# Optimization experiments

Hardware: AMD Instinct MI355X
Metric: run time of the kernel (lower is better)

## Reference

```python
import jax, jax.numpy as jnp
import numpy as np

N, E, NG = 20000, 300000, 64
IN_CH, EDGE_DIM = 64, 7
H1, H2, H3 = 128, 64, 32
HEADS = 4
BN_EPS = 1e-5
NEG_SLOPE = 0.2


def _gat_params(key, in_ch, heads, out_ch, concat):
    ks = jax.random.split(key, 6)
    s_in = 1.0 / np.sqrt(in_ch)
    s_e = 1.0 / np.sqrt(EDGE_DIM)
    W = jax.random.uniform(ks[0], (in_ch, heads * out_ch), minval=-s_in, maxval=s_in)
    a_s = jax.random.uniform(ks[1], (heads, out_ch), minval=-s_in, maxval=s_in)
    a_d = jax.random.uniform(ks[2], (heads, out_ch), minval=-s_in, maxval=s_in)
    We = jax.random.uniform(ks[3], (EDGE_DIM, heads * out_ch), minval=-s_e, maxval=s_e)
    a_e = jax.random.uniform(ks[4], (heads, out_ch), minval=-s_e, maxval=s_e)
    b = jnp.zeros((heads * out_ch,) if concat else (out_ch,), jnp.float32)
    return W, a_s, a_d, We, a_e, b


def _bn_params(key, c):
    k1, k2, k3, k4 = jax.random.split(key, 4)
    g = jax.random.uniform(k1, (c,), minval=0.5, maxval=1.5)
    be = jax.random.normal(k2, (c,)) * 0.1
    rm = jax.random.normal(k3, (c,)) * 0.1
    rv = jax.random.uniform(k4, (c,), minval=0.5, maxval=1.5)
    return g, be, rm, rv


def setup_inputs() -> dict:
    key = jax.random.key(0)
    ks = jax.random.split(key, 12)
    inp = {}
    inp["x"] = jax.random.normal(ks[0], (N, IN_CH), dtype=jnp.float32)
    inp["edge_index"] = jax.random.randint(ks[1], (2, E), 0, N)
    inp["edge_attr"] = jax.random.uniform(ks[2], (E, EDGE_DIM), dtype=jnp.float32)
    inp["batch"] = jnp.sort(jax.random.randint(ks[3], (N,), 0, NG))
    inp["w1"], inp["as1"], inp["ad1"], inp["we1"], inp["ae1"], inp["b1"] = _gat_params(ks[4], IN_CH, HEADS, H1, True)
    inp["g1"], inp["bt1"], inp["rm1"], inp["rv1"] = _bn_params(ks[5], H1 * HEADS)
    inp["w2"], inp["as2"], inp["ad2"], inp["we2"], inp["ae2"], inp["b2"] = _gat_params(ks[6], H1 * HEADS, HEADS, H2, True)
    inp["g2"], inp["bt2"], inp["rm2"], inp["rv2"] = _bn_params(ks[7], H2 * HEADS)
    inp["w3"], inp["as3"], inp["ad3"], inp["we3"], inp["ae3"], inp["b3"] = _gat_params(ks[8], H2 * HEADS, 1, H3, False)
    inp["g3"], inp["bt3"], inp["rm3"], inp["rv3"] = _bn_params(ks[9], H3)
    k10a, k10b = jax.random.split(ks[10])
    s = 1.0 / np.sqrt(H3 * 2)
    inp["lw1"] = jax.random.uniform(k10a, (H3 * 2, 32), minval=-s, maxval=s)
    inp["lb1"] = jax.random.uniform(k10b, (32,), minval=-s, maxval=s)
    k11a, k11b = jax.random.split(ks[11])
    s2 = 1.0 / np.sqrt(32)
    inp["lw2"] = jax.random.uniform(k11a, (32, 1), minval=-s2, maxval=s2)
    inp["lb2"] = jax.random.uniform(k11b, (1,), minval=-s2, maxval=s2)
    return inp


def gat_conv(x, src, dst, eattr, W, a_s, a_d, We, a_e, b, heads, out_ch, concat):
    n = x.shape[0]
    # add self loops; edge_attr for loops = per-destination mean of incoming edge_attr (PyG fill_value='mean')
    deg = jax.ops.segment_sum(jnp.ones_like(eattr[:, 0]), dst, num_segments=n)
    loop_attr = jax.ops.segment_sum(eattr, dst, num_segments=n) / jnp.clip(deg, 1.0)[:, None]
    ar = jnp.arange(n)
    s = jnp.concatenate([src, ar])
    d = jnp.concatenate([dst, ar])
    ea = jnp.concatenate([eattr, loop_attr], axis=0)
    h = (x @ W).reshape(n, heads, out_ch)                       # [N,H,C]
    a_src = jnp.sum(h * a_s, axis=-1)                           # [N,H]
    a_dst = jnp.sum(h * a_d, axis=-1)
    ee = (ea @ We).reshape(-1, heads, out_ch)                   # [Etot,H,C]
    a_edge = jnp.sum(ee * a_e, axis=-1)                         # [Etot,H]
    logit = jax.nn.leaky_relu(a_src[s] + a_dst[d] + a_edge, NEG_SLOPE)
    m = jax.ops.segment_max(logit, d, num_segments=n)           # self loops => every node non-empty
    p = jnp.exp(logit - m[d])
    den = jax.ops.segment_sum(p, d, num_segments=n)
    alpha = p / den[d]                                          # [Etot,H]
    msg = (alpha[..., None] * h[s]).reshape(-1, heads * out_ch)
    out = jax.ops.segment_sum(msg, d, num_segments=n)           # [N,H*C]
    if concat:
        return out + b
    return out.reshape(n, heads, out_ch).mean(axis=1) + b


def bn_eval(x, g, be, rm, rv):
    return (x - rm) * (g / jnp.sqrt(rv + BN_EPS)) + be


def reference(x, edge_index, edge_attr, batch,
              w1, as1, ad1, we1, ae1, b1, g1, bt1, rm1, rv1,
              w2, as2, ad2, we2, ae2, b2, g2, bt2, rm2, rv2,
              w3, as3, ad3, we3, ae3, b3, g3, bt3, rm3, rv3,
              lw1, lb1, lw2, lb2):
    src, dst = edge_index[0], edge_index[1]
    h = jax.nn.relu(bn_eval(gat_conv(x, src, dst, edge_attr, w1, as1, ad1, we1, ae1, b1, HEADS, H1, True), g1, bt1, rm1, rv1))
    h = jax.nn.relu(bn_eval(gat_conv(h, src, dst, edge_attr, w2, as2, ad2, we2, ae2, b2, HEADS, H2, True), g2, bt2, rm2, rv2))
    h = jax.nn.relu(bn_eval(gat_conv(h, src, dst, edge_attr, w3, as3, ad3, we3, ae3, b3, 1, H3, False), g3, bt3, rm3, rv3))
    counts = jax.ops.segment_sum(jnp.ones_like(h[:, 0]), batch, num_segments=NG)
    mean_pool = jax.ops.segment_sum(h, batch, num_segments=NG) / jnp.clip(counts, 1.0)[:, None]
    max_pool = jax.ops.segment_max(h, batch, num_segments=NG)
    max_pool = jnp.where(counts[:, None] > 0, max_pool, 0.0)
    z = jnp.concatenate([mean_pool, max_pool], axis=1)          # [NG, 2*H3]
    z = jax.nn.relu(z @ lw1 + lb1)
    return jax.nn.sigmoid(z @ lw2 + lb2).squeeze(-1)            # [NG]
```

## Files before the change

kernel.cpp:

```cpp
#include <hip/hip_runtime.h>
#include <math.h>

#define NEG_SLOPE 0.2f
#define BN_EPS 1e-5f

typedef __attribute__((ext_vector_type(8))) short bf16x8;
typedef __attribute__((ext_vector_type(4))) float f32x4;
typedef unsigned short u16;
typedef __attribute__((ext_vector_type(4))) unsigned short u16x4;

static __device__ __forceinline__ float leaky(float v) { return v > 0.f ? v : NEG_SLOPE * v; }
static __device__ __forceinline__ float b2f(u16 b) { return __uint_as_float(((unsigned)b) << 16); }
static __device__ __forceinline__ u16 f2b(float f) {
  unsigned u = __float_as_uint(f);
  u += 0x7FFF + ((u >> 16) & 1);
  return (u16)(u >> 16);
}
static __device__ __forceinline__ float sel4(f32x4 v, int hs) {
  float a = (hs & 1) ? v[1] : v[0];
  float b = (hs & 1) ? v[3] : v[2];
  return (hs & 2) ? b : a;
}

__global__ void k_prep(const float* __restrict__ W1, const float* __restrict__ W2, const float* __restrict__ W3,
                       const float* __restrict__ AS1, const float* __restrict__ AD1,
                       const float* __restrict__ WE1, const float* __restrict__ AE1,
                       const float* __restrict__ WE2, const float* __restrict__ AE2,
                       const float* __restrict__ WE3, const float* __restrict__ AE3,
                       u16* __restrict__ Wt1, u16* __restrict__ Wt2, u16* __restrict__ Wt3,
                       float* __restrict__ ws1, float* __restrict__ wd1,
                       float* __restrict__ watt1, float* __restrict__ watt2, float* __restrict__ watt3,
                       int* __restrict__ degInt, int* __restrict__ cursor, int Nn) {
  int idx = blockIdx.x * blockDim.x + threadIdx.x;
  if (idx < 32768) {
    int k = idx >> 9, n = idx & 511;
    Wt1[n * 64 + k] = f2b(W1[idx]);
  } else if (idx < 163840) {
    int i = idx - 32768;
    int k = i >> 8, n = i & 255;
    Wt2[n * 512 + k] = f2b(W2[i]);
  } else if (idx < 172032) {
    int i = idx - 163840;
    int k = i >> 5, n = i & 31;
    Wt3[n * 256 + k] = f2b(W3[i]);
  } else if (idx < 172288) {
    int t = idx - 172032;
    int k = t >> 2, h = t & 3;
    float s1 = 0.f, s2 = 0.f;
    for (int c = 0; c < 128; c++) {
      float w = W1[k * 512 + h * 128 + c];
      s1 += w * AS1[h * 128 + c];
      s2 += w * AD1[h * 128 + c];
    }
    ws1[t] = s1; wd1[t] = s2;
  } else if (idx < 172316) {
    int t = idx - 172288;
    int d = t >> 2, h = t & 3;
    float s = 0.f;
    for (int c = 0; c < 128; c++) s += WE1[d * 512 + h * 128 + c] * AE1[h * 128 + c];
    watt1[t] = s;
  } else if (idx < 172344) {
    int t = idx - 172316;
    int d = t >> 2, h = t & 3;
    float s = 0.f;
    for (int c = 0; c < 64; c++) s += WE2[d * 256 + h * 64 + c] * AE2[h * 64 + c];
    watt2[t] = s;
  } else if (idx < 172351) {
    int d = idx - 172344;
    float s = 0.f;
    for (int c = 0; c < 32; c++) s += WE3[d * 32 + c] * AE3[c];
    watt3[d] = s;
  } else if (idx >= 172352 && idx < 172352 + Nn) {
    degInt[idx - 172352] = 0;
  } else if (idx >= 172352 + Nn && idx < 172352 + 2 * Nn) {
    cursor[idx - 172352 - Nn] = 0;
  }
}

__global__ void k_deg(const int* __restrict__ dst, int* __restrict__ degInt, int E) {
  int e = blockIdx.x * blockDim.x + threadIdx.x;
  if (e < E) atomicAdd(&degInt[dst[e]], 1);
}

__global__ void k_scan(const int* __restrict__ degInt, int* __restrict__ rowStart, int n) {
  __shared__ int sums[1024];
  int tid = threadIdx.x;
  int per = (n + 1023) / 1024;
  int start = tid * per;
  int end = start + per; if (end > n) end = n;
  int s = 0;
  for (int i = start; i < end; i++) s += degInt[i];
  sums[tid] = s;
  __syncthreads();
  for (int off = 1; off < 1024; off <<= 1) {
    int v = (tid >= off) ? sums[tid - off] : 0;
    __syncthreads();
    sums[tid] += v;
    __syncthreads();
  }
  int base = (tid > 0) ? sums[tid - 1] : 0;
  for (int i = start; i < end; i++) { rowStart[i] = base; base += degInt[i]; }
  if (tid == 1023) rowStart[n] = sums[1023];
}

__global__ void k_fill_csr(const int* __restrict__ src, const int* __restrict__ dst,
                           const int* __restrict__ rowStart, int* __restrict__ cursor,
                           int* __restrict__ csrSrc, int* __restrict__ csrEid,
                           int* __restrict__ posE, int E) {
  int e = blockIdx.x * blockDim.x + threadIdx.x;
  if (e >= E) return;
  int d = dst[e];
  int pos = rowStart[d] + atomicAdd(&cursor[d], 1);
  csrSrc[pos] = src[e];
  csrEid[pos] = e;
  posE[e] = pos;
}

__global__ void k_loop_gather(const int* __restrict__ rowStart, const int* __restrict__ csrEid,
                              const float* __restrict__ eattr, float* __restrict__ loopAttr, int Nn) {
  int i = blockIdx.x * blockDim.x + threadIdx.x;
  if (i >= Nn * 7) return;
  int n = i / 7, k = i % 7;
  int r0 = rowStart[n], r1 = rowStart[n + 1];
  float s = 0.f;
  for (int j = r0; j < r1; j++) s += eattr[csrEid[j] * 7 + k];
  loopAttr[i] = s / fmaxf((float)(r1 - r0), 1.0f);
}

__global__ __launch_bounds__(256) void k_cast_attn_x(const float* __restrict__ x, u16* __restrict__ xbf,
                                                     const float* __restrict__ ws, const float* __restrict__ wd,
                                                     float* __restrict__ asrc, float* __restrict__ adst, int Nn) {
  int n = blockIdx.x * 4 + (threadIdx.x >> 6);
  if (n >= Nn) return;
  int lane = threadIdx.x & 63;
  float xv = x[(size_t)n * 64 + lane];
  xbf[(size_t)n * 64 + lane] = f2b(xv);
  f32x4 vs = *(const f32x4*)(ws + lane * 4);
  f32x4 vd = *(const f32x4*)(wd + lane * 4);
  f32x4 s1, s2;
#pragma unroll
  for (int h = 0; h < 4; h++) { s1[h] = xv * vs[h]; s2[h] = xv * vd[h]; }
#pragma unroll
  for (int off = 1; off < 64; off <<= 1) {
#pragma unroll
    for (int h = 0; h < 4; h++) { s1[h] += __shfl_xor(s1[h], off); s2[h] += __shfl_xor(s2[h], off); }
  }
  if (lane == 0) {
    *(f32x4*)(asrc + n * 4) = s1;
    *(f32x4*)(adst + n * 4) = s2;
  }
}

template <int BM, int BN, int WM, int WN, bool EPI, int ATTN_H>
__global__ __launch_bounds__(256) void k_gemm_mfma(const u16* __restrict__ A,
                                                   const u16* __restrict__ Bt,
                                                   u16* __restrict__ Cout,
                                                   int M, int K, int Nc, int lda, int ldc,
                                                   int AzOff, int BzOff, int CzOff,
                                                   const float* __restrict__ bias,
                                                   const float* __restrict__ bng,
                                                   const float* __restrict__ bnb,
                                                   const float* __restrict__ bnrm,
                                                   const float* __restrict__ bnrv,
                                                   const float* __restrict__ a_s,
                                                   const float* __restrict__ a_d,
                                                   float* __restrict__ asrc,
                                                   float* __restrict__ adst) {
  constexpr int BK = 64;
  constexpr int LDT = BK + 8;
  __shared__ u16 As[BM][LDT];
  __shared__ u16 Bs[BN][LDT];
  constexpr int NWN = BN / WN;
  constexpr int M_REP = WM / 16;
  constexpr int N_REP = WN / 16;
  int z = blockIdx.z;
  A += (size_t)z * AzOff;
  Bt += (size_t)z * BzOff;
  Cout += (size_t)z * CzOff;
  if (EPI) {
    bias += (size_t)z * CzOff; bng += (size_t)z * CzOff; bnb += (size_t)z * CzOff;
    bnrm += (size_t)z * CzOff; bnrv += (size_t)z * CzOff;
  }
  int tid = threadIdx.x;
  int wid = tid >> 6, lane = tid & 63;
  int wr = wid / NWN, wc = wid % NWN;
  int bm = blockIdx.x * BM, bn = blockIdx.y * BN;
  int l15 = lane & 15, l4 = lane >> 4;

  f32x4 acc[M_REP][N_REP];
#pragma unroll
  for (int m = 0; m < M_REP; m++)
#pragma unroll
    for (int n = 0; n < N_REP; n++) acc[m][n] = (f32x4){0.f, 0.f, 0.f, 0.f};

  for (int k0 = 0; k0 < K; k0 += BK) {
    constexpr int CHA = BM * BK / 8;
#pragma unroll
    for (int ch0 = 0; ch0 < CHA; ch0 += 256) {
      int ch = ch0 + tid;
      int row = ch >> 3, cc = (ch & 7) * 8;
      int gr = bm + row;
      bf16x8 v = {};
      if (gr < M) v = *(const bf16x8*)(A + (size_t)gr * lda + k0 + cc);
      *(bf16x8*)(&As[row][cc]) = v;
    }
    constexpr int CHB = BN * BK / 8;
#pragma unroll
    for (int ch0 = 0; ch0 < CHB; ch0 += 256) {
      int ch = ch0 + tid;
      int row = ch >> 3, cc = (ch & 7) * 8;
      int gr = bn + row;
      bf16x8 v = {};
      if (gr < Nc) v = *(const bf16x8*)(Bt + (size_t)gr * K + k0 + cc);
      *(bf16x8*)(&Bs[row][cc]) = v;
    }
    __syncthreads();
#pragma unroll
    for (int ks = 0; ks < BK; ks += 32) {
      bf16x8 af[M_REP], bfr[N_REP];
#pragma unroll
      for (int m = 0; m < M_REP; m++)
        af[m] = *(const bf16x8*)(&As[wr * WM + m * 16 + l15][ks + l4 * 8]);
#pragma unroll
      for (int n = 0; n < N_REP; n++)
        bfr[n] = *(const bf16x8*)(&Bs[wc * WN + n * 16 + l15][ks + l4 * 8]);
#pragma unroll
      for (int m = 0; m < M_REP; m++)
#pragma unroll
        for (int n = 0; n < N_REP; n++)
          acc[m][n] = __builtin_amdgcn_mfma_f32_16x16x32_bf16(af[m], bfr[n], acc[m][n], 0, 0, 0);
    }
    __syncthreads();
  }
#pragma unroll
  for (int m = 0; m < M_REP; m++) {
#pragma unroll
    for (int r = 0; r < 4; r++) {
      int grow = bm + wr * WM + m * 16 + l4 * 4 + r;
      if (grow >= M) continue;
#pragma unroll
      for (int n = 0; n < N_REP; n++) {
        int gcol = bn + wc * WN + n * 16 + l15;
        if (gcol >= Nc) continue;
        float v = acc[m][n][r];
        if (EPI) {
          v += bias[gcol];
          v = (v - bnrm[gcol]) * (bng[gcol] * rsqrtf(bnrv[gcol] + BN_EPS)) + bnb[gcol];
          v = fmaxf(v, 0.f);
        }
        Cout[(size_t)grow * ldc + gcol] = f2b(v);
      }
    }
  }
  if (ATTN_H > 0) {
    int h = blockIdx.y * NWN + wc;
#pragma unroll
    for (int m = 0; m < M_REP; m++) {
#pragma unroll
      for (int r = 0; r < 4; r++) {
        float s1 = 0.f, s2 = 0.f;
#pragma unroll
        for (int n = 0; n < N_REP; n++) {
          float av = acc[m][n][r];
          int cc = n * 16 + l15;
          s1 += av * a_s[h * WN + cc];
          s2 += av * a_d[h * WN + cc];
        }
#pragma unroll
        for (int off = 1; off < 16; off <<= 1) { s1 += __shfl_xor(s1, off); s2 += __shfl_xor(s2, off); }
        int grow = bm + wr * WM + m * 16 + l4 * 4 + r;
        if (l15 == 0 && grow < M) {
          asrc[grow * ATTN_H + h] = s1;
          adst[grow * ATTN_H + h] = s2;
        }
      }
    }
  }
}

template <int H>
__global__ void k_edge_logit(const int* __restrict__ src, const int* __restrict__ dst,
                             const float* __restrict__ eattr, const int* __restrict__ posE,
                             const float* __restrict__ asrc, const float* __restrict__ adst,
                             const float* __restrict__ w_att, float* __restrict__ logitC, int E) {
  int e = blockIdx.x * blockDim.x + threadIdx.x;
  if (e >= E) return;
  float ea[7];
#pragma unroll
  for (int d = 0; d < 7; d++) ea[d] = eattr[e * 7 + d];
  int s = src[e], dn = dst[e];
  int pos = posE[e];
  if (H == 4) {
    f32x4 va = *(const f32x4*)(asrc + s * 4);
    f32x4 vd = *(const f32x4*)(adst + dn * 4);
    f32x4 o;
#pragma unroll
    for (int h = 0; h < 4; h++) {
      float ae = 0.f;
#pragma unroll
      for (int d = 0; d < 7; d++) ae += ea[d] * w_att[d * 4 + h];
      o[h] = leaky(va[h] + vd[h] + ae);
    }
    *(f32x4*)(logitC + (size_t)pos * 4) = o;
  } else {
    float ae = 0.f;
#pragma unroll
    for (int d = 0; d < 7; d++) ae += ea[d] * w_att[d];
    logitC[pos] = leaky(asrc[s] + adst[dn] + ae);
  }
}

__global__ __launch_bounds__(256) void k_gather_x(
    const int* __restrict__ rowStart, const int* __restrict__ csrSrc,
    const float* __restrict__ logitC, const float* __restrict__ loopAttr,
    const float* __restrict__ w_att, const float* __restrict__ asrc, const float* __restrict__ adst,
    const u16* __restrict__ xbf, u16* __restrict__ aggOut, int Nn) {
  int wid = threadIdx.x >> 6;
  int n = blockIdx.x * 4 + wid;
  if (n >= Nn) return;
  int lane = threadIdx.x & 63;
  __shared__ float pbuf[4][64 * 4];
  int r0 = rowStart[n], r1 = rowStart[n + 1];

  f32x4 va = *(const f32x4*)(asrc + n * 4);
  f32x4 vd = *(const f32x4*)(adst + n * 4);
  float la[7];
#pragma unroll
  for (int d = 0; d < 7; d++) la[d] = loopAttr[n * 7 + d];
  f32x4 ls;
#pragma unroll
  for (int h = 0; h < 4; h++) {
    float ae = 0.f;
#pragma unroll
    for (int d = 0; d < 7; d++) ae += la[d] * w_att[d * 4 + h];
    ls[h] = leaky(va[h] + vd[h] + ae);
  }

  f32x4 m = ls;
  f32x4 denl = {0.f, 0.f, 0.f, 0.f};
  f32x4 acc = {0.f, 0.f, 0.f, 0.f};

  const f32x4* L4 = (const f32x4*)logitC;
  for (int base = r0; base < r1; base += 64) {
    int slot = base + lane;
    bool valid = slot < r1;
    f32x4 lg = valid ? L4[slot] : (f32x4){-1e30f, -1e30f, -1e30f, -1e30f};
    int srcl = valid ? csrSrc[slot] : 0;
    f32x4 mc = lg;
#pragma unroll
    for (int off = 1; off < 64; off <<= 1) {
#pragma unroll
      for (int h = 0; h < 4; h++) mc[h] = fmaxf(mc[h], __shfl_xor(mc[h], off));
    }
    f32x4 rr;
#pragma unroll
    for (int h = 0; h < 4; h++) {
      float mn = fmaxf(m[h], mc[h]);
      rr[h] = __expf(m[h] - mn);
      m[h] = mn;
      denl[h] *= rr[h];
      acc[h] *= rr[h];
    }
    f32x4 ex;
#pragma unroll
    for (int h = 0; h < 4; h++) ex[h] = valid ? __expf(lg[h] - m[h]) : 0.f;
#pragma unroll
    for (int h = 0; h < 4; h++) denl[h] += ex[h];
    *(f32x4*)(&pbuf[wid][lane * 4]) = ex;
    int nv = r1 - base; if (nv > 64) nv = 64;
    int j = 0;
    for (; j + 1 < nv; j += 2) {
      int s0 = __shfl(srcl, j);
      int s1 = __shfl(srcl, j + 1);
      f32x4 p0 = *(const f32x4*)(&pbuf[wid][j * 4]);
      f32x4 p1 = *(const f32x4*)(&pbuf[wid][(j + 1) * 4]);
      float x0 = b2f(xbf[(size_t)s0 * 64 + lane]);
      float x1 = b2f(xbf[(size_t)s1 * 64 + lane]);
#pragma unroll
      for (int h = 0; h < 4; h++) acc[h] += p0[h] * x0 + p1[h] * x1;
    }
    if (j < nv) {
      int s0 = __shfl(srcl, j);
      f32x4 p0 = *(const f32x4*)(&pbuf[wid][j * 4]);
      float x0 = b2f(xbf[(size_t)s0 * 64 + lane]);
#pragma unroll
      for (int h = 0; h < 4; h++) acc[h] += p0[h] * x0;
    }
  }
  f32x4 exs;
#pragma unroll
  for (int h = 0; h < 4; h++) exs[h] = __expf(ls[h] - m[h]);
  f32x4 den;
#pragma unroll
  for (int h = 0; h < 4; h++) {
    float v = denl[h];
#pragma unroll
    for (int off = 1; off < 64; off <<= 1) v += __shfl_xor(v, off);
    den[h] = v + exs[h];
  }
  {
    float xn = b2f(xbf[(size_t)n * 64 + lane]);
#pragma unroll
    for (int h = 0; h < 4; h++) acc[h] += exs[h] * xn;
  }
#pragma unroll
  for (int h = 0; h < 4; h++) pbuf[wid][h * 64 + lane] = acc[h] / den[h];
  u16x4 ov;
#pragma unroll
  for (int jj = 0; jj < 4; jj++) ov[jj] = f2b(pbuf[wid][lane * 4 + jj]);
  *(u16x4*)(aggOut + (size_t)n * 256 + lane * 4) = ov;
}

template <int C, int CPL>
__global__ __launch_bounds__(256) void k_gather4(
    const int* __restrict__ rowStart, const int* __restrict__ csrSrc,
    const float* __restrict__ logitC, const float* __restrict__ loopAttr,
    const float* __restrict__ w_att, const float* __restrict__ asrc, const float* __restrict__ adst,
    const u16* __restrict__ hbuf, const float* __restrict__ bias,
    const float* __restrict__ bng, const float* __restrict__ bnb,
    const float* __restrict__ bnrm, const float* __restrict__ bnrv,
    u16* __restrict__ outbuf, int Nn) {
  constexpr int HC = 4 * C;
  typedef __attribute__((ext_vector_type(CPL))) unsigned short u16v;
  int wid = threadIdx.x >> 6;
  int n = blockIdx.x * 4 + wid;
  if (n >= Nn) return;
  int lane = threadIdx.x & 63;
  int hs = lane >> 4;
  __shared__ float pbuf[4][64 * 4];
  int r0 = rowStart[n], r1 = rowStart[n + 1];

  f32x4 va = *(const f32x4*)(asrc + n * 4);
  f32x4 vd = *(const f32x4*)(adst + n * 4);
  float la[7];
#pragma unroll
  for (int d = 0; d < 7; d++) la[d] = loopAttr[n * 7 + d];
  f32x4 ls;
#pragma unroll
  for (int h = 0; h < 4; h++) {
    float ae = 0.f;
#pragma unroll
    for (int d = 0; d < 7; d++) ae += la[d] * w_att[d * 4 + h];
    ls[h] = leaky(va[h] + vd[h] + ae);
  }

  f32x4 m = ls;
  f32x4 denl = {0.f, 0.f, 0.f, 0.f};
  float acc[CPL];
#pragma unroll
  for (int jj = 0; jj < CPL; jj++) acc[jj] = 0.f;

  const f32x4* L4 = (const f32x4*)logitC;
  for (int base = r0; base < r1; base += 64) {
    int slot = base + lane;
    bool valid = slot < r1;
    f32x4 lg = valid ? L4[slot] : (f32x4){-1e30f, -1e30f, -1e30f, -1e30f};
    int srcl = valid ? csrSrc[slot] : 0;
    f32x4 mc = lg;
#pragma unroll
    for (int off = 1; off < 64; off <<= 1) {
#pragma unroll
      for (int h = 0; h < 4; h++) mc[h] = fmaxf(mc[h], __shfl_xor(mc[h], off));
    }
    f32x4 rr;
#pragma unroll
    for (int h = 0; h < 4; h++) {
      float mn = fmaxf(m[h], mc[h]);
      rr[h] = __expf(m[h] - mn);
      m[h] = mn;
      denl[h] *= rr[h];
    }
    float rrh = sel4(rr, hs);
#pragma unroll
    for (int jj = 0; jj < CPL; jj++) acc[jj] *= rrh;
    f32x4 ex;
#pragma unroll
    for (int h = 0; h < 4; h++) ex[h] = valid ? __expf(lg[h] - m[h]) : 0.f;
#pragma unroll
    for (int h = 0; h < 4; h++) denl[h] += ex[h];
    *(f32x4*)(&pbuf[wid][lane * 4]) = ex;
    int nv = r1 - base; if (nv > 64) nv = 64;
    int j = 0;
    for (; j + 1 < nv; j += 2) {
      int s0 = __shfl(srcl, j);
      int s1 = __shfl(srcl, j + 1);
      float p0 = pbuf[wid][j * 4 + hs];
      float p1 = pbuf[wid][(j + 1) * 4 + hs];
      u16v h0 = *(const u16v*)(hbuf + (size_t)s0 * HC + lane * CPL);
      u16v h1 = *(const u16v*)(hbuf + (size_t)s1 * HC + lane * CPL);
#pragma unroll
      for (int jj = 0; jj < CPL; jj++) acc[jj] += p0 * b2f(h0[jj]) + p1 * b2f(h1[jj]);
    }
    if (j < nv) {
      int s0 = __shfl(srcl, j);
      float p0 = pbuf[wid][j * 4 + hs];
      u16v h0 = *(const u16v*)(hbuf + (size_t)s0 * HC + lane * CPL);
#pragma unroll
      for (int jj = 0; jj < CPL; jj++) acc[jj] += p0 * b2f(h0[jj]);
    }
  }
  f32x4 exs;
#pragma unroll
  for (int h = 0; h < 4; h++) exs[h] = __expf(ls[h] - m[h]);
  f32x4 den;
#pragma unroll
  for (int h = 0; h < 4; h++) {
    float v = denl[h];
#pragma unroll
    for (int off = 1; off < 64; off <<= 1) v += __shfl_xor(v, off);
    den[h] = v + exs[h];
  }
  {
    float ps = sel4(exs, hs);
    u16v hN = *(const u16v*)(hbuf + (size_t)n * HC + lane * CPL);
#pragma unroll
    for (int jj = 0; jj < CPL; jj++) acc[jj] += ps * b2f(hN[jj]);
  }
  float dh = sel4(den, hs);
  u16v ov;
#pragma unroll
  for (int jj = 0; jj < CPL; jj++) {
    int c = lane * CPL + jj;
    float v = acc[jj] / dh + bias[c];
    v = (v - bnrm[c]) * (bng[c] * rsqrtf(bnrv[c] + BN_EPS)) + bnb[c];
    ov[jj] = f2b(fmaxf(v, 0.f));
  }
  *(u16v*)(outbuf + (size_t)n * HC + lane * CPL) = ov;
}

__global__ __launch_bounds__(256) void k_gather_L3(
    const int* __restrict__ rowStart, const int* __restrict__ csrSrc,
    const float* __restrict__ logitC, const float* __restrict__ loopAttr,
    const float* __restrict__ w_att, const float* __restrict__ asrc, const float* __restrict__ adst,
    const u16* __restrict__ hbuf, const float* __restrict__ bias,
    const float* __restrict__ bng, const float* __restrict__ bnb,
    const float* __restrict__ bnrm, const float* __restrict__ bnrv,
    u16* __restrict__ outbuf, int Nn) {
  int n = blockIdx.x * 4 + (threadIdx.x >> 6);
  if (n >= Nn) return;
  int lane = threadIdx.x & 63;
  int cl = lane & 31, half = lane >> 5;
  int r0 = rowStart[n], r1 = rowStart[n + 1];
  float ae = 0.f;
#pragma unroll
  for (int d = 0; d < 7; d++) ae += loopAttr[n * 7 + d] * w_att[d];
  float ls = leaky(asrc[n] + adst[n] + ae);

  float m = ls;
  for (int j = r0 + lane; j < r1; j += 64) m = fmaxf(m, logitC[j]);
  for (int off = 32; off > 0; off >>= 1) m = fmaxf(m, __shfl_xor(m, off));
  float den = 0.f;
  for (int j = r0 + lane; j < r1; j += 64) den += __expf(logitC[j] - m);
  for (int off = 32; off > 0; off >>= 1) den += __shfl_xor(den, off);
  den += __expf(ls - m);

  float acc = 0.f;
  for (int j = r0 + half; j < r1; j += 2) {
    float p = __expf(logitC[j] - m);
    int s = csrSrc[j];
    acc += p * b2f(hbuf[(size_t)s * 32 + cl]);
  }
  if (half == 0) acc += __expf(ls - m) * b2f(hbuf[(size_t)n * 32 + cl]);
  acc += __shfl_xor(acc, 32);
  if (half == 0) {
    float v = acc / den + bias[cl];
    v = (v - bnrm[cl]) * (bng[cl] * rsqrtf(bnrv[cl] + BN_EPS)) + bnb[cl];
    outbuf[(size_t)n * 32 + cl] = f2b(fmaxf(v, 0.f));
  }
}

__global__ __launch_bounds__(256) void k_pool_mlp(
    const u16* __restrict__ h3, const int* __restrict__ batch, int Nn,
    const float* __restrict__ lw1, const float* __restrict__ lb1,
    const float* __restrict__ lw2, const float* __restrict__ lb2,
    float* __restrict__ out) {
  int g = blockIdx.x;
  int tid = threadIdx.x;
  __shared__ int s_lo, s_hi;
  if (tid == 0) {
    int lo = 0, hi = Nn;
    while (lo < hi) { int mid = (lo + hi) >> 1; if (batch[mid] < g) lo = mid + 1; else hi = mid; }
    s_lo = lo;
    int lo2 = lo, hi2 = Nn;
    while (lo2 < hi2) { int mid = (lo2 + hi2) >> 1; if (batch[mid] < g + 1) lo2 = mid + 1; else hi2 = mid; }
    s_hi = lo2;
  }
  __syncthreads();
  int lo = s_lo, hi = s_hi;
  int c = tid & 31, r = tid >> 5;
  float sum = 0.f, mx = -1e30f;
  for (int n = lo + r; n < hi; n += 8) {
    float v = b2f(h3[(size_t)n * 32 + c]);
    sum += v;
    mx = fmaxf(mx, v);
  }
  __shared__ float ssum[8][32];
  __shared__ float smax[8][32];
  ssum[r][c] = sum;
  smax[r][c] = mx;
  __syncthreads();
  __shared__ float z[64];
  __shared__ float zz1[32];
  if (tid < 32) {
    float s = 0.f, m2 = -1e30f;
#pragma unroll
    for (int rr = 0; rr < 8; rr++) { s += ssum[rr][tid]; m2 = fmaxf(m2, smax[rr][tid]); }
    int cnt = hi - lo;
    z[tid] = s / fmaxf((float)cnt, 1.0f);
    z[32 + tid] = (cnt > 0) ? m2 : 0.f;
  }
  __syncthreads();
  if (tid < 32) {
    float s = lb1[tid];
    for (int k = 0; k < 64; k++) s += z[k] * lw1[k * 32 + tid];
    zz1[tid] = fmaxf(s, 0.f);
  }
  __syncthreads();
  if (tid == 0) {
    float s = lb2[0];
    for (int j = 0; j < 32; j++) s += zz1[j] * lw2[j];
    out[g] = 1.f / (1.f + expf(-s));
  }
}

extern "C" void kernel_launch(void* const* d_in, const int* in_sizes, int n_in,
                              void* d_out, int out_size, void* d_ws, size_t ws_size,
                              hipStream_t stream) {
  const float* x     = (const float*)d_in[0];
  const int*   eidx  = (const int*)d_in[1];
  const float* eattr = (const float*)d_in[2];
  const int*   batch = (const int*)d_in[3];
  int N = in_sizes[0] / 64;
  int E = in_sizes[1] / 2;
  int NG = out_size;
  const int* src = eidx;
  const int* dst = eidx + E;

  const float* W[3]  = {(const float*)d_in[4],  (const float*)d_in[14], (const float*)d_in[24]};
  const float* AS[3] = {(const float*)d_in[5],  (const float*)d_in[15], (const float*)d_in[25]};
  const float* AD[3] = {(const float*)d_in[6],  (const float*)d_in[16], (const float*)d_in[26]};
  const float* WE[3] = {(const float*)d_in[7],  (const float*)d_in[17], (const float*)d_in[27]};
  const float* AE[3] = {(const float*)d_in[8],  (const float*)d_in[18], (const float*)d_in[28]};
  const float* B[3]  = {(const float*)d_in[9],  (const float*)d_in[19], (const float*)d_in[29]};
  const float* G[3]  = {(const float*)d_in[10], (const float*)d_in[20], (const float*)d_in[30]};
  const float* BT[3] = {(const float*)d_in[11], (const float*)d_in[21], (const float*)d_in[31]};
  const float* RM[3] = {(const float*)d_in[12], (const float*)d_in[22], (const float*)d_in[32]};
  const float* RV[3] = {(const float*)d_in[13], (const float*)d_in[23], (const float*)d_in[33]};
  const float* lw1 = (const float*)d_in[34];
  const float* lb1 = (const float*)d_in[35];
  const float* lw2 = (const float*)d_in[36];
  const float* lb2 = (const float*)d_in[37];

  char* wp = (char*)d_ws;
  auto alloc = [&](size_t bytes) -> void* {
    void* p = (void*)wp;
    wp += (bytes + 255) & ~(size_t)255;
    return p;
  };
  u16*   xbf      = (u16*)alloc((size_t)N * 64 * 2);
  u16*   aggB     = (u16*)alloc((size_t)N * 256 * 2);
  u16*   bufH     = (u16*)alloc((size_t)N * 512 * 2);
  u16*   bufA     = (u16*)alloc((size_t)N * 512 * 2);
  u16*   Wt1      = (u16*)alloc((size_t)512 * 64 * 2);
  u16*   Wt2      = (u16*)alloc((size_t)256 * 512 * 2);
  u16*   Wt3      = (u16*)alloc((size_t)32 * 256 * 2);
  int*   degInt   = (int*)alloc((size_t)N * 4);
  int*   cursor   = (int*)alloc((size_t)N * 4);
  int*   rowStart = (int*)alloc((size_t)(N + 1) * 4);
  float* loopAttr = (float*)alloc((size_t)N * 7 * 4);
  int*   csrSrc   = (int*)alloc((size_t)E * 4);
  int*   csrEid   = (int*)alloc((size_t)E * 4);
  int*   posE     = (int*)alloc((size_t)E * 4);
  float* logitC   = (float*)alloc((size_t)E * 4 * 4);
  float* asrc     = (float*)alloc((size_t)N * 4 * 4);
  float* adst     = (float*)alloc((size_t)N * 4 * 4);
  float* watt1    = (float*)alloc(28 * 4);
  float* watt2    = (float*)alloc(28 * 4);
  float* watt3    = (float*)alloc(7 * 4);
  float* ws1      = (float*)alloc(64 * 4 * 4);
  float* wd1      = (float*)alloc(64 * 4 * 4);

  int prepTotal = 172352 + 2 * N;
  k_prep<<<(prepTotal + 255) / 256, 256, 0, stream>>>(
      W[0], W[1], W[2], AS[0], AD[0], WE[0], AE[0], WE[1], AE[1], WE[2], AE[2],
      Wt1, Wt2, Wt3, ws1, wd1, watt1, watt2, watt3, degInt, cursor, N);

  k_deg<<<(E + 255) / 256, 256, 0, stream>>>(dst, degInt, E);
  k_scan<<<1, 1024, 0, stream>>>(degInt, rowStart, N);
  k_fill_csr<<<(E + 255) / 256, 256, 0, stream>>>(src, dst, rowStart, cursor, csrSrc, csrEid, posE, E);
  k_loop_gather<<<(N * 7 + 255) / 256, 256, 0, stream>>>(rowStart, csrEid, eattr, loopAttr, N);

  int gmM = (N + 127) / 128;
  int nb4 = (N + 3) / 4;

  k_cast_attn_x<<<nb4, 256, 0, stream>>>(x, xbf, ws1, wd1, asrc, adst, N);
  k_edge_logit<4><<<(E + 255) / 256, 256, 0, stream>>>(src, dst, eattr, posE, asrc, adst, watt1, logitC, E);
  k_gather_x<<<nb4, 256, 0, stream>>>(rowStart, csrSrc, logitC, loopAttr, watt1, asrc, adst, xbf, aggB, N);
  k_gemm_mfma<128, 128, 64, 64, true, 0><<<dim3(gmM, 1, 4), 256, 0, stream>>>(
      aggB, Wt1, bufA, N, 64, 128, 256, 512, 64, 128 * 64, 128,
      B[0], G[0], BT[0], RM[0], RV[0], nullptr, nullptr, nullptr, nullptr);

  k_gemm_mfma<128, 128, 64, 64, false, 4><<<dim3(gmM, 2, 1), 256, 0, stream>>>(
      bufA, Wt2, bufH, N, 512, 256, 512, 256, 0, 0, 0,
      nullptr, nullptr, nullptr, nullptr, nullptr, AS[1], AD[1], asrc, adst);
  k_edge_logit<4><<<(E + 255) / 256, 256, 0, stream>>>(src, dst, eattr, posE, asrc, adst, watt2, logitC, E);
  k_gather4<64, 4><<<nb4, 256, 0, stream>>>(rowStart, csrSrc, logitC, loopAttr, watt2, asrc, adst,
                                            bufH, B[1], G[1], BT[1], RM[1], RV[1], bufA, N);

  k_gemm_mfma<128, 32, 32, 32, false, 1><<<dim3(gmM, 1, 1), 256, 0, stream>>>(
      bufA, Wt3, bufH, N, 256, 32, 256, 32, 0, 0, 0,
      nullptr, nullptr, nullptr, nullptr, nullptr, AS[2], AD[2], asrc, adst);
  k_edge_logit<1><<<(E + 255) / 256, 256, 0, stream>>>(src, dst, eattr, posE, asrc, adst, watt3, logitC, E);
  k_gather_L3<<<nb4, 256, 0, stream>>>(rowStart, csrSrc, logitC, loopAttr, watt3, asrc, adst,
                                       bufH, B[2], G[2], BT[2], RM[2], RV[2], bufA, N);

  k_pool_mlp<<<NG, 256, 0, stream>>>(bufA, batch, N, lw1, lb1, lw2, lb2, (float*)d_out);
}
```

Before: 285.9 us.

## Precompute edge attention terms once and fuse logit computation into gather kernels

Edge-attribute attention projections for all three layers are computed in one pass and stored in CSR order. The three per-layer edge-logit kernels are removed, and each gather kernel now computes logits on the fly from asrc[src], adst[dst] and the precomputed term. The self-loop attribute mean is rebuilt from the per-edge projected terms, which are linear, and folded in at the end with an online-softmax rescale. This drops the loop_gather kernel, the csrEid array and three launches that each wrote and re-read E x 4 logits. In exchange the gathers do an extra dependent load of asrc per edge, and layer 3 is restructured into a single online-softmax pass.

```diff
diff --git a/kernel.cpp b/kernel.cpp
--- a/kernel.cpp
+++ b/kernel.cpp
@@ -105,26 +105,39 @@
 
 __global__ void k_fill_csr(const int* __restrict__ src, const int* __restrict__ dst,
                            const int* __restrict__ rowStart, int* __restrict__ cursor,
-                           int* __restrict__ csrSrc, int* __restrict__ csrEid,
-                           int* __restrict__ posE, int E) {
+                           int* __restrict__ csrSrc, int* __restrict__ posE, int E) {
   int e = blockIdx.x * blockDim.x + threadIdx.x;
   if (e >= E) return;
   int d = dst[e];
   int pos = rowStart[d] + atomicAdd(&cursor[d], 1);
   csrSrc[pos] = src[e];
-  csrEid[pos] = e;
   posE[e] = pos;
 }
 
-__global__ void k_loop_gather(const int* __restrict__ rowStart, const int* __restrict__ csrEid,
-                              const float* __restrict__ eattr, float* __restrict__ loopAttr, int Nn) {
-  int i = blockIdx.x * blockDim.x + threadIdx.x;
-  if (i >= Nn * 7) return;
-  int n = i / 7, k = i % 7;
-  int r0 = rowStart[n], r1 = rowStart[n + 1];
-  float s = 0.f;
-  for (int j = r0; j < r1; j++) s += eattr[csrEid[j] * 7 + k];
-  loopAttr[i] = s / fmaxf((float)(r1 - r0), 1.0f);
+__global__ void k_ae(const float* __restrict__ eattr, const int* __restrict__ posE,
+                     const float* __restrict__ watt1, const float* __restrict__ watt2,
+                     const float* __restrict__ watt3,
+                     float* __restrict__ ae1, float* __restrict__ ae2, float* __restrict__ ae3, int E) {
+  int e = blockIdx.x * blockDim.x + threadIdx.x;
+  if (e >= E) return;
+  float ea[7];
+#pragma unroll
+  for (int d = 0; d < 7; d++) ea[d] = eattr[e * 7 + d];
+  int pos = posE[e];
+  f32x4 o1, o2;
+#pragma unroll
+  for (int h = 0; h < 4; h++) {
+    float a1 = 0.f, a2 = 0.f;
+#pragma unroll
+    for (int d = 0; d < 7; d++) { a1 += ea[d] * watt1[d * 4 + h]; a2 += ea[d] * watt2[d * 4 + h]; }
+    o1[h] = a1; o2[h] = a2;
+  }
+  float a3 = 0.f;
+#pragma unroll
+  for (int d = 0; d < 7; d++) a3 += ea[d] * watt3[d];
+  *(f32x4*)(ae1 + (size_t)pos * 4) = o1;
+  *(f32x4*)(ae2 + (size_t)pos * 4) = o2;
+  ae3[pos] = a3;
 }
 
 __global__ __launch_bounds__(256) void k_cast_attn_x(const float* __restrict__ x, u16* __restrict__ xbf,
@@ -278,42 +291,9 @@
   }
 }
 
-template <int H>
-__global__ void k_edge_logit(const int* __restrict__ src, const int* __restrict__ dst,
-                             const float* __restrict__ eattr, const int* __restrict__ posE,
-                             const float* __restrict__ asrc, const float* __restrict__ adst,
-                             const float* __restrict__ w_att, float* __restrict__ logitC, int E) {
-  int e = blockIdx.x * blockDim.x + threadIdx.x;
-  if (e >= E) return;
-  float ea[7];
-#pragma unroll
-  for (int d = 0; d < 7; d++) ea[d] = eattr[e * 7 + d];
-  int s = src[e], dn = dst[e];
-  int pos = posE[e];
-  if (H == 4) {
-    f32x4 va = *(const f32x4*)(asrc + s * 4);
-    f32x4 vd = *(const f32x4*)(adst + dn * 4);
-    f32x4 o;
-#pragma unroll
-    for (int h = 0; h < 4; h++) {
-      float ae = 0.f;
-#pragma unroll
-      for (int d = 0; d < 7; d++) ae += ea[d] * w_att[d * 4 + h];
-      o[h] = leaky(va[h] + vd[h] + ae);
-    }
-    *(f32x4*)(logitC + (size_t)pos * 4) = o;
-  } else {
-    float ae = 0.f;
-#pragma unroll
-    for (int d = 0; d < 7; d++) ae += ea[d] * w_att[d];
-    logitC[pos] = leaky(asrc[s] + adst[dn] + ae);
-  }
-}
-
 __global__ __launch_bounds__(256) void k_gather_x(
     const int* __restrict__ rowStart, const int* __restrict__ csrSrc,
-    const float* __restrict__ logitC, const float* __restrict__ loopAttr,
-    const float* __restrict__ w_att, const float* __restrict__ asrc, const float* __restrict__ adst,
+    const float* __restrict__ aeC, const float* __restrict__ asrc, const float* __restrict__ adst,
     const u16* __restrict__ xbf, u16* __restrict__ aggOut, int Nn) {
   int wid = threadIdx.x >> 6;
   int n = blockIdx.x * 4 + wid;
@@ -321,31 +301,27 @@
   int lane = threadIdx.x & 63;
   __shared__ float pbuf[4][64 * 4];
   int r0 = rowStart[n], r1 = rowStart[n + 1];
-
-  f32x4 va = *(const f32x4*)(asrc + n * 4);
-  f32x4 vd = *(const f32x4*)(adst + n * 4);
-  float la[7];
-#pragma unroll
-  for (int d = 0; d < 7; d++) la[d] = loopAttr[n * 7 + d];
-  f32x4 ls;
-#pragma unroll
-  for (int h = 0; h < 4; h++) {
-    float ae = 0.f;
-#pragma unroll
-    for (int d = 0; d < 7; d++) ae += la[d] * w_att[d * 4 + h];
-    ls[h] = leaky(va[h] + vd[h] + ae);
-  }
-
-  f32x4 m = ls;
+  f32x4 vaN = *(const f32x4*)(asrc + n * 4);
+  f32x4 vdN = *(const f32x4*)(adst + n * 4);
+
+  f32x4 m = {-1e30f, -1e30f, -1e30f, -1e30f};
   f32x4 denl = {0.f, 0.f, 0.f, 0.f};
+  f32x4 aes = {0.f, 0.f, 0.f, 0.f};
   f32x4 acc = {0.f, 0.f, 0.f, 0.f};
 
-  const f32x4* L4 = (const f32x4*)logitC;
+  const f32x4* AE4 = (const f32x4*)aeC;
   for (int base = r0; base < r1; base += 64) {
     int slot = base + lane;
     bool valid = slot < r1;
-    f32x4 lg = valid ? L4[slot] : (f32x4){-1e30f, -1e30f, -1e30f, -1e30f};
-    int srcl = valid ? csrSrc[slot] : 0;
+    int srcl = 0;
+    f32x4 lg = {-1e30f, -1e30f, -1e30f, -1e30f};
+    if (valid) {
+      srcl = csrSrc[slot];
+      f32x4 vaS = *(const f32x4*)(asrc + srcl * 4);
+      f32x4 ae = AE4[slot];
+#pragma unroll
+      for (int h = 0; h < 4; h++) { aes[h] += ae[h]; lg[h] = leaky(vaS[h] + vdN[h] + ae[h]); }
+    }
     f32x4 mc = lg;
 #pragma unroll
     for (int off = 1; off < 64; off <<= 1) {
@@ -387,9 +363,21 @@
       for (int h = 0; h < 4; h++) acc[h] += p0[h] * x0;
     }
   }
-  f32x4 exs;
-#pragma unroll
-  for (int h = 0; h < 4; h++) exs[h] = __expf(ls[h] - m[h]);
+  float degf = fmaxf((float)(r1 - r0), 1.0f);
+  f32x4 ls, exs;
+#pragma unroll
+  for (int h = 0; h < 4; h++) {
+    float a = aes[h];
+#pragma unroll
+    for (int off = 1; off < 64; off <<= 1) a += __shfl_xor(a, off);
+    ls[h] = leaky(vaN[h] + vdN[h] + a / degf);
+    float mn = fmaxf(m[h], ls[h]);
+    float sc = __expf(m[h] - mn);
+    m[h] = mn;
+    denl[h] *= sc;
+    acc[h] *= sc;
+    exs[h] = __expf(ls[h] - mn);
+  }
   f32x4 den;
 #pragma unroll
   for (int h = 0; h < 4; h++) {
@@ -414,8 +402,7 @@
 template <int C, int CPL>
 __global__ __launch_bounds__(256) void k_gather4(
     const int* __restrict__ rowStart, const int* __restrict__ csrSrc,
-    const float* __restrict__ logitC, const float* __restrict__ loopAttr,
-    const float* __restrict__ w_att, const float* __restrict__ asrc, const float* __restrict__ adst,
+    const float* __restrict__ aeC, const float* __restrict__ asrc, const float* __restrict__ adst,
     const u16* __restrict__ hbuf, const float* __restrict__ bias,
     const float* __restrict__ bng, const float* __restrict__ bnb,
     const float* __restrict__ bnrm, const float* __restrict__ bnrv,
@@ -429,33 +416,29 @@
   int hs = lane >> 4;
   __shared__ float pbuf[4][64 * 4];
   int r0 = rowStart[n], r1 = rowStart[n + 1];
-
-  f32x4 va = *(const f32x4*)(asrc + n * 4);
-  f32x4 vd = *(const f32x4*)(adst + n * 4);
-  float la[7];
-#pragma unroll
-  for (int d = 0; d < 7; d++) la[d] = loopAttr[n * 7 + d];
-  f32x4 ls;
-#pragma unroll
-  for (int h = 0; h < 4; h++) {
-    float ae = 0.f;
-#pragma unroll
-    for (int d = 0; d < 7; d++) ae += la[d] * w_att[d * 4 + h];
-    ls[h] = leaky(va[h] + vd[h] + ae);
-  }
-
-  f32x4 m = ls;
+  f32x4 vaN = *(const f32x4*)(asrc + n * 4);
+  f32x4 vdN = *(const f32x4*)(adst + n * 4);
+
+  f32x4 m = {-1e30f, -1e30f, -1e30f, -1e30f};
   f32x4 denl = {0.f, 0.f, 0.f, 0.f};
+  f32x4 aes = {0.f, 0.f, 0.f, 0.f};
   float acc[CPL];
 #pragma unroll
   for (int jj = 0; jj < CPL; jj++) acc[jj] = 0.f;
 
-  const f32x4* L4 = (const f32x4*)logitC;
+  const f32x4* AE4 = (const f32x4*)aeC;
   for (int base = r0; base < r1; base += 64) {
     int slot = base + lane;
     bool valid = slot < r1;
-    f32x4 lg = valid ? L4[slot] : (f32x4){-1e30f, -1e30f, -1e30f, -1e30f};
-    int srcl = valid ? csrSrc[slot] : 0;
+    int srcl = 0;
+    f32x4 lg = {-1e30f, -1e30f, -1e30f, -1e30f};
+    if (valid) {
+      srcl = csrSrc[slot];
+      f32x4 vaS = *(const f32x4*)(asrc + srcl * 4);
+      f32x4 ae = AE4[slot];
+#pragma unroll
+      for (int h = 0; h < 4; h++) { aes[h] += ae[h]; lg[h] = leaky(vaS[h] + vdN[h] + ae[h]); }
+    }
     f32x4 mc = lg;
 #pragma unroll
     for (int off = 1; off < 64; off <<= 1) {
@@ -499,9 +482,23 @@
       for (int jj = 0; jj < CPL; jj++) acc[jj] += p0 * b2f(h0[jj]);
     }
   }
-  f32x4 exs;
-#pragma unroll
-  for (int h = 0; h < 4; h++) exs[h] = __expf(ls[h] - m[h]);
+  float degf = fmaxf((float)(r1 - r0), 1.0f);
+  f32x4 ls, exs, scv;
+#pragma unroll
+  for (int h = 0; h < 4; h++) {
+    float a = aes[h];
+#pragma unroll
+    for (int off = 1; off < 64; off <<= 1) a += __shfl_xor(a, off);
+    ls[h] = leaky(vaN[h] + vdN[h] + a / degf);
+    float mn = fmaxf(m[h], ls[h]);
+    scv[h] = __expf(m[h] - mn);
+    m[h] = mn;
+    denl[h] *= scv[h];
+    exs[h] = __expf(ls[h] - mn);
+  }
+  float sch = sel4(scv, hs);
+#pragma unroll
+  for (int jj = 0; jj < CPL; jj++) acc[jj] *= sch;
   f32x4 den;
 #pragma unroll
   for (int h = 0; h < 4; h++) {
@@ -530,37 +527,63 @@
 
 __global__ __launch_bounds__(256) void k_gather_L3(
     const int* __restrict__ rowStart, const int* __restrict__ csrSrc,
-    const float* __restrict__ logitC, const float* __restrict__ loopAttr,
-    const float* __restrict__ w_att, const float* __restrict__ asrc, const float* __restrict__ adst,
+    const float* __restrict__ ae3, const float* __restrict__ asrc, const float* __restrict__ adst,
     const u16* __restrict__ hbuf, const float* __restrict__ bias,
     const float* __restrict__ bng, const float* __restrict__ bnb,
     const float* __restrict__ bnrm, const float* __restrict__ bnrv,
     u16* __restrict__ outbuf, int Nn) {
-  int n = blockIdx.x * 4 + (threadIdx.x >> 6);
+  int wid = threadIdx.x >> 6;
+  int n = blockIdx.x * 4 + wid;
   if (n >= Nn) return;
   int lane = threadIdx.x & 63;
   int cl = lane & 31, half = lane >> 5;
+  __shared__ float pbuf[4][64];
   int r0 = rowStart[n], r1 = rowStart[n + 1];
-  float ae = 0.f;
-#pragma unroll
-  for (int d = 0; d < 7; d++) ae += loopAttr[n * 7 + d] * w_att[d];
-  float ls = leaky(asrc[n] + adst[n] + ae);
-
-  float m = ls;
-  for (int j = r0 + lane; j < r1; j += 64) m = fmaxf(m, logitC[j]);
-  for (int off = 32; off > 0; off >>= 1) m = fmaxf(m, __shfl_xor(m, off));
-  float den = 0.f;
-  for (int j = r0 + lane; j < r1; j += 64) den += __expf(logitC[j] - m);
-  for (int off = 32; off > 0; off >>= 1) den += __shfl_xor(den, off);
-  den += __expf(ls - m);
-
-  float acc = 0.f;
-  for (int j = r0 + half; j < r1; j += 2) {
-    float p = __expf(logitC[j] - m);
-    int s = csrSrc[j];
-    acc += p * b2f(hbuf[(size_t)s * 32 + cl]);
-  }
-  if (half == 0) acc += __expf(ls - m) * b2f(hbuf[(size_t)n * 32 + cl]);
+  float vaN = asrc[n], vdN = adst[n];
+
+  float m = -1e30f, denl = 0.f, aes = 0.f, acc = 0.f;
+  for (int base = r0; base < r1; base += 64) {
+    int slot = base + lane;
+    bool valid = slot < r1;
+    int srcl = 0;
+    float lg = -1e30f;
+    if (valid) {
+      srcl = csrSrc[slot];
+      float ae = ae3[slot];
+      aes += ae;
+      lg = leaky(asrc[srcl] + vdN + ae);
+    }
+    float mc = lg;
+#pragma unroll
+    for (int off = 1; off < 64; off <<= 1) mc = fmaxf(mc, __shfl_xor(mc, off));
+    float mn = fmaxf(m, mc);
+    float sc = __expf(m - mn);
+    m = mn;
+    denl *= sc;
+    acc *= sc;
+    float ex = valid ? __expf(lg - m) : 0.f;
+    denl += ex;
+    pbuf[wid][lane] = ex;
+    int nv = r1 - base; if (nv > 64) nv = 64;
+    for (int j = half; j < nv; j += 2) {
+      float p = pbuf[wid][j];
+      int s = __shfl(srcl, j);
+      acc += p * b2f(hbuf[(size_t)s * 32 + cl]);
+    }
+  }
+#pragma unroll
+  for (int off = 1; off < 64; off <<= 1) aes += __shfl_xor(aes, off);
+  float degf = fmaxf((float)(r1 - r0), 1.0f);
+  float ls = leaky(vaN + vdN + aes / degf);
+  float mn = fmaxf(m, ls);
+  float sc = __expf(m - mn);
+  denl *= sc;
+  acc *= sc;
+  float exs = __expf(ls - mn);
+#pragma unroll
+  for (int off = 1; off < 64; off <<= 1) denl += __shfl_xor(denl, off);
+  float den = denl + exs;
+  if (half == 0) acc += exs * b2f(hbuf[(size_t)n * 32 + cl]);
   acc += __shfl_xor(acc, 32);
   if (half == 0) {
     float v = acc / den + bias[cl];
@@ -667,11 +690,11 @@
   int*   degInt   = (int*)alloc((size_t)N * 4);
   int*   cursor   = (int*)alloc((size_t)N * 4);
   int*   rowStart = (int*)alloc((size_t)(N + 1) * 4);
-  float* loopAttr = (float*)alloc((size_t)N * 7 * 4);
   int*   csrSrc   = (int*)alloc((size_t)E * 4);
-  int*   csrEid   = (int*)alloc((size_t)E * 4);
   int*   posE     = (int*)alloc((size_t)E * 4);
-  float* logitC   = (float*)alloc((size_t)E * 4 * 4);
+  float* ae1      = (float*)alloc((size_t)E * 4 * 4);
+  float* ae2      = (float*)alloc((size_t)E * 4 * 4);
+  float* ae3buf   = (float*)alloc((size_t)E * 4);
   float* asrc     = (float*)alloc((size_t)N * 4 * 4);
   float* adst     = (float*)alloc((size_t)N * 4 * 4);
   float* watt1    = (float*)alloc(28 * 4);
@@ -687,15 +710,14 @@
 
   k_deg<<<(E + 255) / 256, 256, 0, stream>>>(dst, degInt, E);
   k_scan<<<1, 1024, 0, stream>>>(degInt, rowStart, N);
-  k_fill_csr<<<(E + 255) / 256, 256, 0, stream>>>(src, dst, rowStart, cursor, csrSrc, csrEid, posE, E);
-  k_loop_gather<<<(N * 7 + 255) / 256, 256, 0, stream>>>(rowStart, csrEid, eattr, loopAttr, N);
+  k_fill_csr<<<(E + 255) / 256, 256, 0, stream>>>(src, dst, rowStart, cursor, csrSrc, posE, E);
+  k_ae<<<(E + 255) / 256, 256, 0, stream>>>(eattr, posE, watt1, watt2, watt3, ae1, ae2, ae3buf, E);
 
   int gmM = (N + 127) / 128;
   int nb4 = (N + 3) / 4;
 
   k_cast_attn_x<<<nb4, 256, 0, stream>>>(x, xbf, ws1, wd1, asrc, adst, N);
-  k_edge_logit<4><<<(E + 255) / 256, 256, 0, stream>>>(src, dst, eattr, posE, asrc, adst, watt1, logitC, E);
-  k_gather_x<<<nb4, 256, 0, stream>>>(rowStart, csrSrc, logitC, loopAttr, watt1, asrc, adst, xbf, aggB, N);
+  k_gather_x<<<nb4, 256, 0, stream>>>(rowStart, csrSrc, ae1, asrc, adst, xbf, aggB, N);
   k_gemm_mfma<128, 128, 64, 64, true, 0><<<dim3(gmM, 1, 4), 256, 0, stream>>>(
       aggB, Wt1, bufA, N, 64, 128, 256, 512, 64, 128 * 64, 128,
       B[0], G[0], BT[0], RM[0], RV[0], nullptr, nullptr, nullptr, nullptr);
@@ -703,15 +725,13 @@
   k_gemm_mfma<128, 128, 64, 64, false, 4><<<dim3(gmM, 2, 1), 256, 0, stream>>>(
       bufA, Wt2, bufH, N, 512, 256, 512, 256, 0, 0, 0,
       nullptr, nullptr, nullptr, nullptr, nullptr, AS[1], AD[1], asrc, adst);
-  k_edge_logit<4><<<(E + 255) / 256, 256, 0, stream>>>(src, dst, eattr, posE, asrc, adst, watt2, logitC, E);
-  k_gather4<64, 4><<<nb4, 256, 0, stream>>>(rowStart, csrSrc, logitC, loopAttr, watt2, asrc, adst,
+  k_gather4<64, 4><<<nb4, 256, 0, stream>>>(rowStart, csrSrc, ae2, asrc, adst,
                                             bufH, B[1], G[1], BT[1], RM[1], RV[1], bufA, N);
 
   k_gemm_mfma<128, 32, 32, 32, false, 1><<<dim3(gmM, 1, 1), 256, 0, stream>>>(
       bufA, Wt3, bufH, N, 256, 32, 256, 32, 0, 0, 0,
       nullptr, nullptr, nullptr, nullptr, nullptr, AS[2], AD[2], asrc, adst);
-  k_edge_logit<1><<<(E + 255) / 256, 256, 0, stream>>>(src, dst, eattr, posE, asrc, adst, watt3, logitC, E);
-  k_gather_L3<<<nb4, 256, 0, stream>>>(rowStart, csrSrc, logitC, loopAttr, watt3, asrc, adst,
+  k_gather_L3<<<nb4, 256, 0, stream>>>(rowStart, csrSrc, ae3buf, asrc, adst,
                                        bufH, B[2], G[2], BT[2], RM[2], RV[2], bufA, N);
 
   k_pool_mlp<<<NG, 256, 0, stream>>>(bufA, batch, N, lw1, lb1, lw2, lb2, (float*)d_out);
```

Measured after the change: 265.3 us. 1.08x faster.
